# Optimization experiments

Measured on AMD Instinct MI355X. Metric: run time of the kernel, lower is better.

Reference implementation:

```python
import jax, jax.numpy as jnp
import numpy as np

B, N, C, R, E = 8, 4096, 128, 16, 65536


def setup_inputs() -> dict:
    key = jax.random.key(0)
    ks = jax.random.split(key, 8)
    node_features = jax.random.normal(ks[0], (B, N, C), dtype=jnp.float32)
    edge_index = jax.random.randint(ks[1], (B, 2, E), 0, N, dtype=jnp.int64)
    edge_type = jax.random.randint(ks[2], (B, E), 0, R, dtype=jnp.int64)
    s = 1.0 / np.sqrt(C)
    rel_weight = jax.random.uniform(ks[3], (R, C, C), jnp.float32, -s, s)
    root_weight = jax.random.uniform(ks[4], (C, C), jnp.float32, -s, s)
    rgcn_bias = jnp.zeros((C,), jnp.float32)
    lin_weight = jax.random.uniform(ks[5], (C, 1), jnp.float32, -s, s)
    lin_bias = jnp.zeros((1,), jnp.float32)
    return {
        'node_features': node_features,
        'edge_index': edge_index,
        'edge_type': edge_type,
        'rel_weight': rel_weight,
        'root_weight': root_weight,
        'rgcn_bias': rgcn_bias,
        'lin_weight': lin_weight,
        'lin_bias': lin_bias,
    }


def _rgcn_score(node_features, edge_index, edge_type, rel_weight, root_weight,
                rgcn_bias, lin_weight, lin_bias):
    # Flatten batch of graphs into one big disjoint graph (as batch_rgcn does).
    x = node_features.reshape(B * N, C)
    offs = (jnp.arange(B, dtype=edge_index.dtype) * N)[:, None, None]  # (B,1,1)
    ei = (edge_index + offs).transpose(1, 0, 2).reshape(2, B * E)  # (2, B*E)
    et = edge_type.reshape(B * E)
    src, dst = ei[0], ei[1]

    x_src = x[src]  # (B*E, C) gathered source features
    # root transform + bias (RGCNConv root_weight + bias)
    out = x @ root_weight + rgcn_bias  # (B*N, C)
    # per-relation mean aggregation; mean(W_r x_j) == W_r mean(x_j)
    for r in range(R):
        mask = (et == r).astype(x.dtype)  # (B*E,)
        s = jax.ops.segment_sum(x_src * mask[:, None], dst, num_segments=B * N)
        cnt = jax.ops.segment_sum(mask, dst, num_segments=B * N)
        mean = jnp.where(cnt[:, None] > 0, s / jnp.maximum(cnt, 1.0)[:, None], 0.0)
        out = out + mean @ rel_weight[r]

    out = jax.nn.relu(out)  # dropout is identity at eval
    scores = (out @ lin_weight + lin_bias).reshape(B, N)
    return scores


def reference(node_features, edge_index, edge_type, rel_weight, root_weight,
              rgcn_bias, lin_weight, lin_bias):
    return _rgcn_score(node_features, edge_index, edge_type, rel_weight,
                       root_weight, rgcn_bias, lin_weight, lin_bias)
```

## Files before the change

kernel.cpp:

```cpp
#include <hip/hip_runtime.h>

#define BB 8
#define NN 4096
#define CC 128
#define RR 16
#define EE 65536
#define NNODES 32768
#define NEDGES 524288
#define KTOT   2176
#define LDP    80
#define BCAP   60
#define GEMMB  4352

typedef unsigned short ushort_t;
typedef short bf16x8 __attribute__((ext_vector_type(8)));
typedef float f32x4 __attribute__((ext_vector_type(4)));

__device__ __forceinline__ unsigned short f2b(float f) {
    unsigned u = __builtin_bit_cast(unsigned, f);
    unsigned r = (u + 0x7fffu + ((u >> 16) & 1u)) >> 16;
    return (unsigned short)r;
}
__device__ __forceinline__ float b2f(unsigned short s) {
    return __builtin_bit_cast(float, (unsigned)s << 16);
}
__device__ __forceinline__ float ldf(const void* p, int j, int isbf) {
    return isbf ? b2f(((const ushort_t*)p)[j]) : ((const float*)p)[j];
}
__device__ __forceinline__ int ldi(const int* p, int j, int is64) {
    return p[j << is64];
}

__device__ __forceinline__ int probe_isbf(const ushort_t* xf) {
    int t = threadIdx.x & 63;
    int bad = 0;
    for (int j = t; j < 512; j += 64) {
        unsigned e = (xf[j] >> 7) & 0xffu;
        if (e >= 160u) bad = 1;
    }
    return __ballot(bad) == 0ull;
}

__global__ __launch_bounds__(256) void prep_k(const void* __restrict__ x,
                                              const void* __restrict__ relw,
                                              const void* __restrict__ rootw,
                                              const int* __restrict__ ei,
                                              const int* __restrict__ et,
                                              ushort_t* __restrict__ Xb,
                                              ushort_t* __restrict__ WT,
                                              int* __restrict__ dcnt,
                                              int* __restrict__ flags) {
    int bx = blockIdx.x, t = threadIdx.x;
    if (bx < 2048) {
        int isbf = probe_isbf((const ushort_t*)x);
        int tid = bx * 256 + t;
        if (isbf) {
            ((uint4*)Xb)[tid] = ((const uint4*)x)[tid];
        } else {
            const float4* xf = (const float4*)x;
            float4 a = xf[2 * tid], b = xf[2 * tid + 1];
            ushort4 o0, o1;
            o0.x = f2b(a.x); o0.y = f2b(a.y); o0.z = f2b(a.z); o0.w = f2b(a.w);
            o1.x = f2b(b.x); o1.y = f2b(b.y); o1.z = f2b(b.z); o1.w = f2b(b.w);
            ((ushort4*)Xb)[2 * tid] = o0; ((ushort4*)Xb)[2 * tid + 1] = o1;
        }
    } else if (bx < 3136) {
        int isbf = probe_isbf((const ushort_t*)x);
        int tid = (bx - 2048) * 256 + t;
        int nglob = tid >> 7, k = tid & 127;
        int jb = nglob >> 7, n = nglob & 127;
        float v = (jb == 0) ? ldf(rootw, k * 128 + n, isbf)
                            : ldf(relw, ((jb - 1) << 14) + k * 128 + n, isbf);
        WT[tid] = f2b(v);
    } else if (bx < 3168) {
        int tid = (bx - 3136) * 256 + t;
        ((uint4*)dcnt)[tid] = make_uint4(0, 0, 0, 0);
    } else {
        if (t < 64) {
            int isbf = probe_isbf((const ushort_t*)x);
            int a = (t < 16) ? ei[2 * t + 1] : 0;
            int b = (t < 16) ? et[2 * t + 1] : 0;
            unsigned long long ma = __ballot(a != 0);
            unsigned long long mb = __ballot(b != 0);
            if (t == 0) {
                flags[0] = isbf;
                flags[1] = (ma == 0ull);
                flags[2] = (mb == 0ull);
            }
        }
    }
}

__global__ __launch_bounds__(256) void ge_k(const ushort_t* __restrict__ Xb,
                                            const ushort_t* __restrict__ WT,
                                            ushort_t* __restrict__ Y,
                                            const int* __restrict__ ei,
                                            const int* __restrict__ et,
                                            int* __restrict__ dcnt,
                                            int* __restrict__ bucket,
                                            const int* __restrict__ flags) {
    __shared__ ushort_t As[128][LDP];
    __shared__ ushort_t Bs[128][LDP];
    int bx = blockIdx.x, t = threadIdx.x;
    if (bx >= GEMMB) {
        int w64i = flags[1], w64t = flags[2];
        int tid = (bx - GEMMB) * 256 + t;
        int b = tid >> 16, e = tid & 65535;
        int src = ldi(ei, (b * 2) * EE + e, w64i);
        int dst = ldi(ei, (b * 2 + 1) * EE + e, w64i);
        int r = ldi(et, tid, w64t);
        int gd = (b << 12) + dst;
        int pos = atomicAdd(&dcnt[gd], 1);
        if (pos < BCAP)
            bucket[gd * BCAP + pos] = (((b << 12) + src) << 4) | r;
        return;
    }
    int m0 = (bx & 255) * 128, n0 = (bx >> 8) * 128;
    int wave = t >> 6, lane = t & 63, lrow = lane & 15, lq = lane >> 4;
    int wm = (wave >> 1) * 64, wn = (wave & 1) * 64;
    f32x4 acc[4][4] = {};

    for (int kt = 0; kt < 2; ++kt) {
        #pragma unroll
        for (int i = 0; i < 4; ++i) {
            int c = t + i * 256;
            int row = c >> 3, c8 = c & 7;
            uint4 va = *(const uint4*)(Xb + (size_t)(m0 + row) * 128 + kt * 64 + c8 * 8);
            *(uint4*)(&As[row][c8 * 8]) = va;
            uint4 vb = *(const uint4*)(WT + (size_t)(n0 + row) * 128 + kt * 64 + c8 * 8);
            *(uint4*)(&Bs[row][c8 * 8]) = vb;
        }
        __syncthreads();
        #pragma unroll
        for (int ks = 0; ks < 2; ++ks) {
            int k0 = ks * 32 + lq * 8;
            bf16x8 a[4], b[4];
            #pragma unroll
            for (int mi = 0; mi < 4; ++mi) a[mi] = *(const bf16x8*)(&As[wm + mi * 16 + lrow][k0]);
            #pragma unroll
            for (int ni = 0; ni < 4; ++ni) b[ni] = *(const bf16x8*)(&Bs[wn + ni * 16 + lrow][k0]);
            #pragma unroll
            for (int mi = 0; mi < 4; ++mi)
                #pragma unroll
                for (int ni = 0; ni < 4; ++ni)
                    acc[mi][ni] = __builtin_amdgcn_mfma_f32_16x16x32_bf16(a[mi], b[ni], acc[mi][ni], 0, 0, 0);
        }
        __syncthreads();
    }
    #pragma unroll
    for (int mi = 0; mi < 4; ++mi)
        #pragma unroll
        for (int rg = 0; rg < 4; ++rg) {
            int row = wm + mi * 16 + lq * 4 + rg;
            ushort_t* yr = Y + (size_t)(m0 + row) * KTOT + n0 + wn;
            #pragma unroll
            for (int ni = 0; ni < 4; ++ni)
                yr[ni * 16 + lrow] = f2b(acc[mi][ni][rg]);
        }
}

__global__ __launch_bounds__(128) void agg_score_k(const ushort_t* __restrict__ Y,
                                                   const int* __restrict__ dcnt,
                                                   const int* __restrict__ bucket,
                                                   const void* __restrict__ bias,
                                                   const void* __restrict__ linw,
                                                   const void* __restrict__ linb,
                                                   void* __restrict__ out,
                                                   const int* __restrict__ flags) {
    int i = blockIdx.x, t = threadIdx.x;
    int isbf = flags[0];
    __shared__ int scnt[RR];
    __shared__ float inv[RR];
    int nc = dcnt[i]; if (nc > BCAP) nc = BCAP;
    const int* bk = bucket + i * BCAP;
    if (t < RR) scnt[t] = 0;
    __syncthreads();
    if (t < nc) atomicAdd(&scnt[bk[t] & 15], 1);
    __syncthreads();
    if (t < RR) inv[t] = (scnt[t] > 0) ? 1.0f / (float)scnt[t] : 0.0f;
    __syncthreads();

    float acc = b2f(Y[(size_t)i * KTOT + t]) + ldf(bias, t, isbf);
    int e = 0;
    for (; e + 7 < nc; e += 8) {
        int v[8]; float y[8];
        #pragma unroll
        for (int j = 0; j < 8; ++j) v[j] = bk[e + j];
        #pragma unroll
        for (int j = 0; j < 8; ++j)
            y[j] = b2f(Y[(size_t)(v[j] >> 4) * KTOT + CC + ((v[j] & 15) << 7) + t]);
        #pragma unroll
        for (int j = 0; j < 8; ++j) acc += inv[v[j] & 15] * y[j];
    }
    for (; e + 3 < nc; e += 4) {
        int v0 = bk[e], v1 = bk[e + 1], v2 = bk[e + 2], v3 = bk[e + 3];
        float y0 = b2f(Y[(size_t)(v0 >> 4) * KTOT + CC + ((v0 & 15) << 7) + t]);
        float y1 = b2f(Y[(size_t)(v1 >> 4) * KTOT + CC + ((v1 & 15) << 7) + t]);
        float y2 = b2f(Y[(size_t)(v2 >> 4) * KTOT + CC + ((v2 & 15) << 7) + t]);
        float y3 = b2f(Y[(size_t)(v3 >> 4) * KTOT + CC + ((v3 & 15) << 7) + t]);
        acc += inv[v0 & 15] * y0 + inv[v1 & 15] * y1 + inv[v2 & 15] * y2 + inv[v3 & 15] * y3;
    }
    for (; e < nc; ++e) {
        int v = bk[e];
        acc += inv[v & 15] * b2f(Y[(size_t)(v >> 4) * KTOT + CC + ((v & 15) << 7) + t]);
    }
    float val = fmaxf(acc, 0.f) * ldf(linw, t, isbf);
    for (int o = 32; o > 0; o >>= 1) val += __shfl_down(val, o, 64);
    __shared__ float red[2];
    if ((t & 63) == 0) red[t >> 6] = val;
    __syncthreads();
    if (t == 0) {
        float res = red[0] + red[1] + ldf(linb, 0, isbf);
        if (isbf) ((ushort_t*)out)[i] = f2b(res);
        else      ((float*)out)[i] = res;
    }
}

extern "C" void kernel_launch(void* const* d_in, const int* in_sizes, int n_in,
                              void* d_out, int out_size, void* d_ws, size_t ws_size,
                              hipStream_t stream) {
    const void* x     = d_in[0];
    const int*  ei    = (const int*)d_in[1];
    const int*  et    = (const int*)d_in[2];
    const void* relw  = d_in[3];
    const void* rootw = d_in[4];
    const void* bias  = d_in[5];
    const void* linw  = d_in[6];
    const void* linb  = d_in[7];

    const size_t WS_NEED = 159547904;
    if (ws_size < WS_NEED) return;

    char* ws = (char*)d_ws;
    ushort_t* Y      = (ushort_t*)(ws);
    ushort_t* Xb     = (ushort_t*)(ws + 142606336);
    ushort_t* WT     = (ushort_t*)(ws + 150994944);
    int*      dcnt   = (int*)(ws + 151552000);
    int*      bucket = (int*)(ws + 151683072);
    int*      flags  = (int*)(ws + 159547392);

    prep_k<<<3169, 256, 0, stream>>>(x, relw, rootw, ei, et, Xb, WT, dcnt, flags);
    ge_k<<<GEMMB + 2048, 256, 0, stream>>>(Xb, WT, Y, ei, et, dcnt, bucket, flags);
    agg_score_k<<<NNODES, 128, 0, stream>>>(Y, dcnt, bucket, bias, linw, linb, d_out, flags);
}
```

Measured before the change: 174.7 us.

## Aggregate neighbors before transform and fuse GEMM, aggregation, scoring into one kernel

Switches from transform-then-gather (a GEMM producing a 32768x2176 Y buffer that is then gathered per edge) to gather-then-transform. Each block of 128 nodes computes per-relation mean features in registers, writes them into shared memory, runs MFMA against each relation's weight tile, and fuses bias, ReLU and the linear score into the epilogue. Edge bucketing moves into the prep kernel and the counter clear into a memset. This removes the large Y write and reread, but the fused kernel runs only 256 blocks with one block per SM. Each block also rescans all bucketed edges once per relation, so parallelism is low and the per-block serial work is long.

```diff
diff --git a/kernel.cpp b/kernel.cpp
--- a/kernel.cpp
+++ b/kernel.cpp
@@ -7,10 +7,8 @@
 #define EE 65536
 #define NNODES 32768
 #define NEDGES 524288
-#define KTOT   2176
-#define LDP    80
 #define BCAP   60
-#define GEMMB  4352
+#define LDB    136
 
 typedef unsigned short ushort_t;
 typedef short bf16x8 __attribute__((ext_vector_type(8)));
@@ -41,19 +39,40 @@
     return __ballot(bad) == 0ull;
 }
 
-__global__ __launch_bounds__(256) void prep_k(const void* __restrict__ x,
-                                              const void* __restrict__ relw,
-                                              const void* __restrict__ rootw,
-                                              const int* __restrict__ ei,
-                                              const int* __restrict__ et,
-                                              ushort_t* __restrict__ Xb,
-                                              ushort_t* __restrict__ WT,
-                                              int* __restrict__ dcnt,
-                                              int* __restrict__ flags) {
+__global__ __launch_bounds__(256) void pe_k(const void* __restrict__ x,
+                                            const void* __restrict__ relw,
+                                            const void* __restrict__ rootw,
+                                            const int* __restrict__ ei,
+                                            const int* __restrict__ et,
+                                            ushort_t* __restrict__ Xb,
+                                            ushort_t* __restrict__ WT,
+                                            int* __restrict__ dcnt,
+                                            int* __restrict__ bucket,
+                                            int* __restrict__ flags) {
     int bx = blockIdx.x, t = threadIdx.x;
     if (bx < 2048) {
+        __shared__ int sw64i, sw64t;
+        if (t < 64) {
+            int a = (t < 16) ? ei[2 * t + 1] : 0;
+            int b = (t < 16) ? et[2 * t + 1] : 0;
+            unsigned long long ma = __ballot(a != 0);
+            unsigned long long mb = __ballot(b != 0);
+            if (t == 0) { sw64i = (ma == 0ull); sw64t = (mb == 0ull); }
+        }
+        __syncthreads();
+        int w64i = sw64i, w64t = sw64t;
+        int tid = bx * 256 + t;
+        int b = tid >> 16, e = tid & 65535;
+        int src = ldi(ei, (b * 2) * EE + e, w64i);
+        int dst = ldi(ei, (b * 2 + 1) * EE + e, w64i);
+        int r = ldi(et, tid, w64t);
+        int gd = (b << 12) + dst;
+        int pos = atomicAdd(&dcnt[gd], 1);
+        if (pos < BCAP)
+            bucket[gd * BCAP + pos] = (((b << 12) + src) << 4) | r;
+    } else if (bx < 4096) {
         int isbf = probe_isbf((const ushort_t*)x);
-        int tid = bx * 256 + t;
+        int tid = (bx - 2048) * 256 + t;
         if (isbf) {
             ((uint4*)Xb)[tid] = ((const uint4*)x)[tid];
         } else {
@@ -64,75 +83,114 @@
             o1.x = f2b(b.x); o1.y = f2b(b.y); o1.z = f2b(b.z); o1.w = f2b(b.w);
             ((ushort4*)Xb)[2 * tid] = o0; ((ushort4*)Xb)[2 * tid + 1] = o1;
         }
-    } else if (bx < 3136) {
+    } else if (bx < 5184) {
         int isbf = probe_isbf((const ushort_t*)x);
-        int tid = (bx - 2048) * 256 + t;
+        int tid = (bx - 4096) * 256 + t;
         int nglob = tid >> 7, k = tid & 127;
         int jb = nglob >> 7, n = nglob & 127;
         float v = (jb == 0) ? ldf(rootw, k * 128 + n, isbf)
                             : ldf(relw, ((jb - 1) << 14) + k * 128 + n, isbf);
         WT[tid] = f2b(v);
-    } else if (bx < 3168) {
-        int tid = (bx - 3136) * 256 + t;
-        ((uint4*)dcnt)[tid] = make_uint4(0, 0, 0, 0);
     } else {
         if (t < 64) {
             int isbf = probe_isbf((const ushort_t*)x);
-            int a = (t < 16) ? ei[2 * t + 1] : 0;
-            int b = (t < 16) ? et[2 * t + 1] : 0;
-            unsigned long long ma = __ballot(a != 0);
-            unsigned long long mb = __ballot(b != 0);
-            if (t == 0) {
-                flags[0] = isbf;
-                flags[1] = (ma == 0ull);
-                flags[2] = (mb == 0ull);
-            }
-        }
-    }
-}
-
-__global__ __launch_bounds__(256) void ge_k(const ushort_t* __restrict__ Xb,
-                                            const ushort_t* __restrict__ WT,
-                                            ushort_t* __restrict__ Y,
-                                            const int* __restrict__ ei,
-                                            const int* __restrict__ et,
-                                            int* __restrict__ dcnt,
-                                            int* __restrict__ bucket,
-                                            const int* __restrict__ flags) {
-    __shared__ ushort_t As[128][LDP];
-    __shared__ ushort_t Bs[128][LDP];
-    int bx = blockIdx.x, t = threadIdx.x;
-    if (bx >= GEMMB) {
-        int w64i = flags[1], w64t = flags[2];
-        int tid = (bx - GEMMB) * 256 + t;
-        int b = tid >> 16, e = tid & 65535;
-        int src = ldi(ei, (b * 2) * EE + e, w64i);
-        int dst = ldi(ei, (b * 2 + 1) * EE + e, w64i);
-        int r = ldi(et, tid, w64t);
-        int gd = (b << 12) + dst;
-        int pos = atomicAdd(&dcnt[gd], 1);
-        if (pos < BCAP)
-            bucket[gd * BCAP + pos] = (((b << 12) + src) << 4) | r;
-        return;
-    }
-    int m0 = (bx & 255) * 128, n0 = (bx >> 8) * 128;
+            if (t == 0) flags[0] = isbf;
+        }
+    }
+}
+
+__global__ __launch_bounds__(256, 1) void rgcn_k(const ushort_t* __restrict__ Xb,
+                                                 const ushort_t* __restrict__ WT,
+                                                 const int* __restrict__ dcnt,
+                                                 const int* __restrict__ bucket,
+                                                 const void* __restrict__ bias,
+                                                 const void* __restrict__ linw,
+                                                 const void* __restrict__ linb,
+                                                 void* __restrict__ out,
+                                                 const int* __restrict__ flags) {
+    __shared__ ushort_t As[128][LDB];
+    __shared__ ushort_t Bs[128][LDB];
+    __shared__ int bkc[128][BCAP];
+    __shared__ int ncs[128];
+    __shared__ float scorebuf[128];
+    int t = threadIdx.x;
+    int m0 = blockIdx.x * 128;
+    int isbf = flags[0];
+    int node2 = t >> 1, half = t & 1;
+
+    if (t < 128) scorebuf[t] = 0.f;
+    if (half == 0) {
+        int nc = dcnt[m0 + node2];
+        ncs[node2] = (nc > BCAP) ? BCAP : nc;
+    }
+    __syncthreads();
+    {
+        int nc = ncs[node2];
+        const int* bk = bucket + (size_t)(m0 + node2) * BCAP;
+        for (int j = half; j < nc; j += 2) bkc[node2][j] = bk[j];
+    }
+    __syncthreads();
+
     int wave = t >> 6, lane = t & 63, lrow = lane & 15, lq = lane >> 4;
     int wm = (wave >> 1) * 64, wn = (wave & 1) * 64;
     f32x4 acc[4][4] = {};
 
-    for (int kt = 0; kt < 2; ++kt) {
+    for (int jb = 0; jb < 17; ++jb) {
         #pragma unroll
-        for (int i = 0; i < 4; ++i) {
+        for (int i = 0; i < 8; ++i) {
             int c = t + i * 256;
-            int row = c >> 3, c8 = c & 7;
-            uint4 va = *(const uint4*)(Xb + (size_t)(m0 + row) * 128 + kt * 64 + c8 * 8);
-            *(uint4*)(&As[row][c8 * 8]) = va;
-            uint4 vb = *(const uint4*)(WT + (size_t)(n0 + row) * 128 + kt * 64 + c8 * 8);
-            *(uint4*)(&Bs[row][c8 * 8]) = vb;
+            int row = c >> 4, c16 = c & 15;
+            uint4 vb = *(const uint4*)(WT + ((size_t)(jb * 128 + row) << 7) + c16 * 8);
+            *(uint4*)(&Bs[row][c16 * 8]) = vb;
+        }
+        if (jb == 0) {
+            #pragma unroll
+            for (int i = 0; i < 8; ++i) {
+                int c = t + i * 256;
+                int row = c >> 4, c16 = c & 15;
+                uint4 va = *(const uint4*)(Xb + ((size_t)(m0 + row) << 7) + c16 * 8);
+                *(uint4*)(&As[row][c16 * 8]) = va;
+            }
+        } else {
+            int r = jb - 1;
+            float f[64];
+            #pragma unroll
+            for (int k = 0; k < 64; ++k) f[k] = 0.f;
+            int nc = ncs[node2];
+            int c = 0;
+            for (int j = 0; j < nc; ++j) {
+                int v = bkc[node2][j];
+                if ((v & 15) == r) {
+                    ++c;
+                    const ushort_t* xr = Xb + (((size_t)(v >> 4)) << 7) + half * 64;
+                    #pragma unroll
+                    for (int q = 0; q < 8; ++q) {
+                        uint4 u = *(const uint4*)(xr + q * 8);
+                        f[q * 8 + 0] += __builtin_bit_cast(float, u.x << 16);
+                        f[q * 8 + 1] += __builtin_bit_cast(float, u.x & 0xffff0000u);
+                        f[q * 8 + 2] += __builtin_bit_cast(float, u.y << 16);
+                        f[q * 8 + 3] += __builtin_bit_cast(float, u.y & 0xffff0000u);
+                        f[q * 8 + 4] += __builtin_bit_cast(float, u.z << 16);
+                        f[q * 8 + 5] += __builtin_bit_cast(float, u.z & 0xffff0000u);
+                        f[q * 8 + 6] += __builtin_bit_cast(float, u.w << 16);
+                        f[q * 8 + 7] += __builtin_bit_cast(float, u.w & 0xffff0000u);
+                    }
+                }
+            }
+            float inv = (c > 0) ? 1.0f / (float)c : 0.0f;
+            #pragma unroll
+            for (int q = 0; q < 8; ++q) {
+                uint4 o;
+                o.x = ((unsigned)f2b(f[q * 8 + 1] * inv) << 16) | f2b(f[q * 8 + 0] * inv);
+                o.y = ((unsigned)f2b(f[q * 8 + 3] * inv) << 16) | f2b(f[q * 8 + 2] * inv);
+                o.z = ((unsigned)f2b(f[q * 8 + 5] * inv) << 16) | f2b(f[q * 8 + 4] * inv);
+                o.w = ((unsigned)f2b(f[q * 8 + 7] * inv) << 16) | f2b(f[q * 8 + 6] * inv);
+                *(uint4*)(&As[node2][half * 64 + q * 8]) = o;
+            }
         }
         __syncthreads();
         #pragma unroll
-        for (int ks = 0; ks < 2; ++ks) {
+        for (int ks = 0; ks < 4; ++ks) {
             int k0 = ks * 32 + lq * 8;
             bf16x8 a[4], b[4];
             #pragma unroll
@@ -147,72 +205,33 @@
         }
         __syncthreads();
     }
+
+    float bcol[4], lcol[4];
+    #pragma unroll
+    for (int ni = 0; ni < 4; ++ni) {
+        int col = wn + ni * 16 + lrow;
+        bcol[ni] = ldf(bias, col, isbf);
+        lcol[ni] = ldf(linw, col, isbf);
+    }
     #pragma unroll
     for (int mi = 0; mi < 4; ++mi)
         #pragma unroll
         for (int rg = 0; rg < 4; ++rg) {
-            int row = wm + mi * 16 + lq * 4 + rg;
-            ushort_t* yr = Y + (size_t)(m0 + row) * KTOT + n0 + wn;
+            float s = 0.f;
             #pragma unroll
             for (int ni = 0; ni < 4; ++ni)
-                yr[ni * 16 + lrow] = f2b(acc[mi][ni][rg]);
-        }
-}
-
-__global__ __launch_bounds__(128) void agg_score_k(const ushort_t* __restrict__ Y,
-                                                   const int* __restrict__ dcnt,
-                                                   const int* __restrict__ bucket,
-                                                   const void* __restrict__ bias,
-                                                   const void* __restrict__ linw,
-                                                   const void* __restrict__ linb,
-                                                   void* __restrict__ out,
-                                                   const int* __restrict__ flags) {
-    int i = blockIdx.x, t = threadIdx.x;
-    int isbf = flags[0];
-    __shared__ int scnt[RR];
-    __shared__ float inv[RR];
-    int nc = dcnt[i]; if (nc > BCAP) nc = BCAP;
-    const int* bk = bucket + i * BCAP;
-    if (t < RR) scnt[t] = 0;
+                s += fmaxf(acc[mi][ni][rg] + bcol[ni], 0.f) * lcol[ni];
+            s += __shfl_down(s, 8, 16);
+            s += __shfl_down(s, 4, 16);
+            s += __shfl_down(s, 2, 16);
+            s += __shfl_down(s, 1, 16);
+            if (lrow == 0) atomicAdd(&scorebuf[wm + mi * 16 + lq * 4 + rg], s);
+        }
     __syncthreads();
-    if (t < nc) atomicAdd(&scnt[bk[t] & 15], 1);
-    __syncthreads();
-    if (t < RR) inv[t] = (scnt[t] > 0) ? 1.0f / (float)scnt[t] : 0.0f;
-    __syncthreads();
-
-    float acc = b2f(Y[(size_t)i * KTOT + t]) + ldf(bias, t, isbf);
-    int e = 0;
-    for (; e + 7 < nc; e += 8) {
-        int v[8]; float y[8];
-        #pragma unroll
-        for (int j = 0; j < 8; ++j) v[j] = bk[e + j];
-        #pragma unroll
-        for (int j = 0; j < 8; ++j)
-            y[j] = b2f(Y[(size_t)(v[j] >> 4) * KTOT + CC + ((v[j] & 15) << 7) + t]);
-        #pragma unroll
-        for (int j = 0; j < 8; ++j) acc += inv[v[j] & 15] * y[j];
-    }
-    for (; e + 3 < nc; e += 4) {
-        int v0 = bk[e], v1 = bk[e + 1], v2 = bk[e + 2], v3 = bk[e + 3];
-        float y0 = b2f(Y[(size_t)(v0 >> 4) * KTOT + CC + ((v0 & 15) << 7) + t]);
-        float y1 = b2f(Y[(size_t)(v1 >> 4) * KTOT + CC + ((v1 & 15) << 7) + t]);
-        float y2 = b2f(Y[(size_t)(v2 >> 4) * KTOT + CC + ((v2 & 15) << 7) + t]);
-        float y3 = b2f(Y[(size_t)(v3 >> 4) * KTOT + CC + ((v3 & 15) << 7) + t]);
-        acc += inv[v0 & 15] * y0 + inv[v1 & 15] * y1 + inv[v2 & 15] * y2 + inv[v3 & 15] * y3;
-    }
-    for (; e < nc; ++e) {
-        int v = bk[e];
-        acc += inv[v & 15] * b2f(Y[(size_t)(v >> 4) * KTOT + CC + ((v & 15) << 7) + t]);
-    }
-    float val = fmaxf(acc, 0.f) * ldf(linw, t, isbf);
-    for (int o = 32; o > 0; o >>= 1) val += __shfl_down(val, o, 64);
-    __shared__ float red[2];
-    if ((t & 63) == 0) red[t >> 6] = val;
-    __syncthreads();
-    if (t == 0) {
-        float res = red[0] + red[1] + ldf(linb, 0, isbf);
-        if (isbf) ((ushort_t*)out)[i] = f2b(res);
-        else      ((float*)out)[i] = res;
+    if (t < 128) {
+        float res = scorebuf[t] + ldf(linb, 0, isbf);
+        if (isbf) ((ushort_t*)out)[m0 + t] = f2b(res);
+        else      ((float*)out)[m0 + t] = res;
     }
 }
 
@@ -228,18 +247,17 @@
     const void* linw  = d_in[6];
     const void* linb  = d_in[7];
 
-    const size_t WS_NEED = 159547904;
+    const size_t WS_NEED = 16941312;
     if (ws_size < WS_NEED) return;
 
     char* ws = (char*)d_ws;
-    ushort_t* Y      = (ushort_t*)(ws);
-    ushort_t* Xb     = (ushort_t*)(ws + 142606336);
-    ushort_t* WT     = (ushort_t*)(ws + 150994944);
-    int*      dcnt   = (int*)(ws + 151552000);
-    int*      bucket = (int*)(ws + 151683072);
-    int*      flags  = (int*)(ws + 159547392);
-
-    prep_k<<<3169, 256, 0, stream>>>(x, relw, rootw, ei, et, Xb, WT, dcnt, flags);
-    ge_k<<<GEMMB + 2048, 256, 0, stream>>>(Xb, WT, Y, ei, et, dcnt, bucket, flags);
-    agg_score_k<<<NNODES, 128, 0, stream>>>(Y, dcnt, bucket, bias, linw, linb, d_out, flags);
-}
+    ushort_t* Xb     = (ushort_t*)(ws);
+    ushort_t* WT     = (ushort_t*)(ws + 8388608);
+    int*      dcnt   = (int*)(ws + 8945664);
+    int*      bucket = (int*)(ws + 9076736);
+    int*      flags  = (int*)(ws + 16941056);
+
+    hipMemsetAsync(dcnt, 0, 131072, stream);
+    pe_k<<<5185, 256, 0, stream>>>(x, relw, rootw, ei, et, Xb, WT, dcnt, bucket, flags);
+    rgcn_k<<<256, 256, 0, stream>>>(Xb, WT, dcnt, bucket, bias, linw, linb, d_out, flags);
+}
```

Measured after the change: 324.1 us. +85.5%, slower.
